# Performance work log

Measured on AMD Instinct MI355X. Metric: run time of the kernel, lower is better.

## Reference

```python
import jax, jax.numpy as jnp
import numpy as np

B, S, HID, H = 2, 2048, 2048, 16
D = HID // H  # 128 head dim
SCALE = 1.0 / np.sqrt(D)


def setup_inputs() -> dict:
    key = jax.random.key(0)
    ks = jax.random.split(key, 10)
    w = lambda k, shp: (jax.random.normal(k, shp, jnp.float32) * 0.02)
    x = jax.random.normal(ks[0], (B, S, HID), jnp.float32)
    mask = jnp.tril(jnp.ones((S, S), jnp.bool_))[None, None]  # causal [1,1,S,S]
    return {
        "x": x,
        "mask": mask,
        "Wq": w(ks[1], (HID, HID)), "bq": w(ks[2], (HID,)),
        "Wk": w(ks[3], (D, HID)),   "bk": w(ks[4], (D,)),
        "Wv": w(ks[5], (D, HID)),   "bv": w(ks[6], (D,)),
        "Wo": w(ks[7], (HID, HID)), "bo": w(ks[8], (HID,)),
    }


def reference(x, mask, Wq, bq, Wk, bk, Wv, bv, Wo, bo):
    b, s, _ = x.shape
    # projections (torch Linear: x @ W.T + b)
    q = (x @ Wq.T + bq).reshape(b, s, H, D).transpose(0, 2, 1, 3)  # [B,H,S,D]
    k = x @ Wk.T + bk  # [B,S,D] single KV head
    v = x @ Wv.T + bv  # [B,S,D]
    scores = jnp.einsum("bhqd,bkd->bhqk", q, k) * SCALE  # [B,H,S,S]
    scores = jnp.where(mask, scores, -jnp.inf)
    attn = jax.nn.softmax(scores, axis=-1)
    out = jnp.einsum("bhqk,bkd->bhqd", attn, v)  # [B,H,S,D]
    out = out.transpose(0, 2, 1, 3).reshape(b, s, HID)
    return out @ Wo.T + bo
```

## Files before the change

### kernel.cpp

```cpp
#include <hip/hip_runtime.h>


#define S_LEN 2048
#define HID_  2048
#define D_    128
#define NQKV  2304

typedef __attribute__((ext_vector_type(8))) short bf16x8;
typedef __attribute__((ext_vector_type(4))) float f32x4;
typedef __attribute__((ext_vector_type(16))) float f32x16;

__device__ __forceinline__ unsigned short f2b(float f) {
  union { float f; unsigned int u; } a; a.f = f;
  unsigned int u = a.u;
  return (unsigned short)((u + 0x7fffu + ((u >> 16) & 1u)) >> 16);
}

__device__ __forceinline__ float b2f(unsigned short s) {
  union { unsigned int u; float f; } a; a.u = ((unsigned int)s) << 16;
  return a.f;
}

__device__ __forceinline__ void load_lds16(const void* g, void* l) {
  __builtin_amdgcn_global_load_lds(
      (const __attribute__((address_space(1))) void*)g,
      (__attribute__((address_space(3))) void*)l, 16, 0, 0);
}

__device__ __forceinline__ f32x4 mfma16(bf16x8 a, bf16x8 b, f32x4 c) {
  return __builtin_amdgcn_mfma_f32_16x16x32_bf16(a, b, c, 0, 0, 0);
}

__device__ __forceinline__ f32x16 mfma32(bf16x8 a, bf16x8 b, f32x16 c) {
  return __builtin_amdgcn_mfma_f32_32x32x16_bf16(a, b, c, 0, 0, 0);
}

__device__ __forceinline__ unsigned int cvtpk(float lo, float hi) {
  unsigned int r;
  asm volatile("v_cvt_pk_bf16_f32 %0, %1, %2" : "=v"(r) : "v"(lo), "v"(hi));
  return r;
}


__global__ void cast_f32_bf16_k(const float* __restrict__ in,
                                unsigned short* __restrict__ out, int n4) {
  const int idx = blockIdx.x * 256 + threadIdx.x;
  if (idx < n4) {
    const float4 v = ((const float4*)in)[idx];
    ushort4 o;
    o.x = f2b(v.x); o.y = f2b(v.y); o.z = f2b(v.z); o.w = f2b(v.w);
    ((ushort4*)out)[idx] = o;
  }
}

__global__ void build_wcat_k(const float* __restrict__ Wq,
                             const float* __restrict__ Wk,
                             const float* __restrict__ Wv,
                             const float* __restrict__ bq,
                             const float* __restrict__ bk,
                             const float* __restrict__ bv,
                             unsigned short* __restrict__ Wcat,
                             float* __restrict__ bcat,
                             float* __restrict__ Kmax) {
  const int idx = blockIdx.x * 256 + threadIdx.x;
  const int i = idx * 4;
  const int row = i >> 11;
  const int col = i & 2047;
  const float* src;
  if (row < 2048)      src = Wq + (size_t)row * 2048 + col;
  else if (row < 2176) src = Wk + (size_t)(row - 2048) * 2048 + col;
  else                 src = Wv + (size_t)(row - 2176) * 2048 + col;
  const float4 v = *(const float4*)src;
  ushort4 o;
  o.x = f2b(v.x); o.y = f2b(v.y); o.z = f2b(v.z); o.w = f2b(v.w);
  *(ushort4*)(Wcat + i) = o;
  if (idx < NQKV)
    bcat[idx] = (idx < 2048) ? bq[idx] : (idx < 2176) ? bk[idx - 2048] : bv[idx - 2176];
  if (idx < 2) Kmax[idx] = 0.f;
}

__global__ __launch_bounds__(256)
void transpose_v(const unsigned short* __restrict__ QKV,
                 unsigned short* __restrict__ Vt) {
  __shared__ unsigned short tile[64][136];
  const int tid = threadIdx.x;
  const int s0  = blockIdx.x * 64;
  const int b   = blockIdx.y;
  const int row = tid >> 2;
  const int cb  = (tid & 3) * 32;
  const unsigned short* src = QKV + (size_t)(b * S_LEN + s0 + row) * NQKV + 2176 + cb;
#pragma unroll
  for (int i = 0; i < 4; ++i)
    *(bf16x8*)&tile[row][cb + i * 8] = *(const bf16x8*)(src + i * 8);
  __syncthreads();
  const int d  = tid >> 1;
  const int sc = (tid & 1) * 32;
  unsigned short* dst = Vt + ((size_t)b * D_ + d) * S_LEN + s0 + sc;
#pragma unroll
  for (int i = 0; i < 4; ++i) {
    bf16x8 vv;
#pragma unroll
    for (int e = 0; e < 8; ++e) vv[e] = tile[sc + i * 8 + e][d];
    *(bf16x8*)(dst + i * 8) = vv;
  }
}

__global__ __launch_bounds__(256)
void kmax_k(const unsigned short* __restrict__ QKV, float* __restrict__ Kmax) {
  __shared__ float red[256];
  const int tid = threadIdx.x;
  const int b = blockIdx.x >> 3;
  const int s = (blockIdx.x & 7) * 256 + tid;
  const unsigned short* kp = QKV + (size_t)(b * S_LEN + s) * NQKV + 2048;
  float sum = 0.f;
#pragma unroll
  for (int i = 0; i < 16; ++i) {
    bf16x8 v = *(const bf16x8*)(kp + i * 8);
#pragma unroll
    for (int e = 0; e < 8; ++e) { const float f = b2f((unsigned short)v[e]); sum += f * f; }
  }
  red[tid] = sum;
  __syncthreads();
  for (int off = 128; off > 0; off >>= 1) {
    if (tid < off) red[tid] = fmaxf(red[tid], red[tid + off]);
    __syncthreads();
  }
  if (tid == 0) atomicMax((unsigned int*)(Kmax + b), __float_as_uint(red[0]));
}


template <int OUT_F32>
__global__ __launch_bounds__(256)
void gemm_nt(const unsigned short* __restrict__ A,
             const unsigned short* __restrict__ Bm,
             const float* __restrict__ bias,
             void* __restrict__ Cv,
             int M, int N, int K) {
  __shared__ unsigned short As[128 * 32];
  __shared__ unsigned short Bs[128 * 32];
  const int tid  = threadIdx.x;
  const int lane = tid & 63;
  const int wv   = tid >> 6;
  const int wr   = wv >> 1, wc = wv & 1;
  const int g    = lane >> 4, r = lane & 15;
  const int m0   = blockIdx.y * 128;
  const int n0   = blockIdx.x * 128;

  const unsigned short* ga0 = A  + (size_t)(m0 + (tid >> 2)) * K + (tid & 3) * 8;
  const unsigned short* ga1 = ga0 + (size_t)64 * K;
  const unsigned short* gb0 = Bm + (size_t)(n0 + (tid >> 2)) * K + (tid & 3) * 8;
  const unsigned short* gb1 = gb0 + (size_t)64 * K;

  f32x4 acc[4][4] = {};

  for (int k0 = 0; k0 < K; k0 += 32) {
    __syncthreads();
    load_lds16(ga0 + k0, &As[tid * 8]);
    load_lds16(ga1 + k0, &As[2048 + tid * 8]);
    load_lds16(gb0 + k0, &Bs[tid * 8]);
    load_lds16(gb1 + k0, &Bs[2048 + tid * 8]);
    __syncthreads();
    bf16x8 af[4], bfr[4];
#pragma unroll
    for (int i = 0; i < 4; ++i)
      af[i] = *(const bf16x8*)&As[(wr * 64 + i * 16 + r) * 32 + g * 8];
#pragma unroll
    for (int i = 0; i < 4; ++i)
      bfr[i] = *(const bf16x8*)&Bs[(wc * 64 + i * 16 + r) * 32 + g * 8];
#pragma unroll
    for (int i = 0; i < 4; ++i)
#pragma unroll
      for (int j = 0; j < 4; ++j)
        acc[i][j] = mfma16(af[i], bfr[j], acc[i][j]);
  }

#pragma unroll
  for (int i = 0; i < 4; ++i) {
    const int row = m0 + wr * 64 + i * 16 + g * 4;
#pragma unroll
    for (int j = 0; j < 4; ++j) {
      const int col = n0 + wc * 64 + j * 16 + r;
      const float bb = bias[col];
#pragma unroll
      for (int e = 0; e < 4; ++e) {
        const float v = acc[i][j][e] + bb;
        if (OUT_F32) ((float*)Cv)[(size_t)(row + e) * N + col] = v;
        else ((unsigned short*)Cv)[(size_t)(row + e) * N + col] = f2b(v);
      }
    }
  }
}


__global__ __launch_bounds__(256, 2)
void mqa_attn(const unsigned short* __restrict__ QKV,
              const unsigned short* __restrict__ Vt,
              const float* __restrict__ Kmax,
              unsigned short* __restrict__ Ob) {
  __shared__ __align__(16) char Ks[2][64 * 256];
  __shared__ __align__(16) char Vs[2][64 * 256];

  const int tid  = threadIdx.x;
  const int lane = tid & 63;
  const int wv   = tid >> 6;
  const int ln   = lane & 31;
  const int hi   = lane >> 5;
  const int x    = blockIdx.x;
  const int lo   = x & 255;
  const int b    = lo >> 7;
  const int hq   = (lo >> 5) & 3;
  const int qtl  = lo & 31;
  const int qt   = (x < 256) ? qtl : 63 - qtl;
  const int h    = hq * 4 + wv;
  const int qw   = qt * 32;
  const int nt   = (qt >> 1) + 1;

  bf16x8 qf[8];
  {
    const unsigned short* qp =
        QKV + (size_t)(b * S_LEN + qw + ln) * NQKV + h * D_ + hi * 8;
#pragma unroll
    for (int ch = 0; ch < 8; ++ch) qf[ch] = *(const bf16x8*)(qp + ch * 16);
  }

  const float sscale = 0.08838834764831845f * 1.4426950408889634f;
  float qn2 = 0.f;
#pragma unroll
  for (int ch = 0; ch < 8; ++ch)
#pragma unroll
    for (int e = 0; e < 8; ++e) {
      const float qv = b2f((unsigned short)qf[ch][e]);
      qn2 += qv * qv;
    }
  qn2 += __shfl_xor(qn2, 32);
  const float m0c = sqrtf(qn2) * sqrtf(Kmax[b]) * sscale + 1.0f;

  const char* kbc = (const char*)(QKV + (size_t)(b * S_LEN) * NQKV + 2048);
  const char* vbc = (const char*)(Vt + (size_t)b * D_ * S_LEN);

  f32x16 acc[4] = {};
  float accl = 0.f;

#define STAGE(bufi, t)                                                         \
  {                                                                            \
    const int kv0_ = (t) * 64;                                                 \
    _Pragma("unroll")                                                          \
    for (int i_ = 0; i_ < 4; ++i_) {                                           \
      const int ch_ = tid + 256 * i_;                                          \
      const int kr_ = ch_ >> 4;                                                \
      const int kg_ = (ch_ & 15) ^ (kr_ & 15);                                 \
      load_lds16(kbc + (size_t)(kv0_ + kr_) * (NQKV * 2) + kg_ * 16,           \
                 Ks[bufi] + ch_ * 16);                                         \
      const int vg_ = (ch_ & 15) ^ (kr_ & 15);                                 \
      const int vd_ = kr_ * 2 + (vg_ >> 3);                                    \
      load_lds16(vbc + (size_t)vd_ * (S_LEN * 2) + kv0_ * 2 + (vg_ & 7) * 16,  \
                 Vs[bufi] + ch_ * 16);                                         \
    }                                                                          \
  }

  STAGE(0, 0);
  int cur = 0;

  for (int t = 0; t < nt; ++t) {
    __syncthreads();
    if (t + 1 < nt) STAGE(cur ^ 1, t + 1);

    const char* ksb = Ks[cur];
    const char* vsb = Vs[cur];
    const int kv0 = t * 64;
    const bool last = (t == nt - 1);
    const bool doUp = (kv0 + 32 <= qw + 31);
    cur ^= 1;

    f32x16 s0 = {}, s1 = {};
    __builtin_amdgcn_s_setprio(1);
#pragma unroll
    for (int ch = 0; ch < 8; ++ch) {
      const int slot0 = (2 * ch + hi) ^ (ln & 15);
      const bf16x8 kf0 = *(const bf16x8*)(ksb + ln * 256 + slot0 * 16);
      s0 = mfma32(kf0, qf[ch], s0);
      if (doUp) {
        const bf16x8 kf1 = *(const bf16x8*)(ksb + (32 + ln) * 256 + slot0 * 16);
        s1 = mfma32(kf1, qf[ch], s1);
      }
    }
    __builtin_amdgcn_s_setprio(0);

    bf16x8 pa0, pa1, pa2, pa3;
    float p[16];

#define SOFTMAX(sv, kvtbase)                                                   \
    _Pragma("unroll")                                                          \
    for (int r = 0; r < 16; ++r) {                                             \
      float e = sv[r] * sscale - m0c;                                          \
      if (last) {                                                              \
        const int kva = (kvtbase) + (r & 3) + 8 * (r >> 2) + 4 * hi;           \
        e = (kva <= qw + ln) ? e : -__builtin_inff();                          \
      }                                                                        \
      const float pv_ = __builtin_amdgcn_exp2f(e);                             \
      p[r] = pv_; accl += pv_;                                                 \
    }

#define PACK2(fa, fb)                                                          \
    {                                                                          \
      const unsigned int A0 = cvtpk(p[0], p[1]),   A1 = cvtpk(p[2], p[3]);     \
      const unsigned int B0 = cvtpk(p[4], p[5]),   B1 = cvtpk(p[6], p[7]);     \
      const unsigned int C0 = cvtpk(p[8], p[9]),   C1 = cvtpk(p[10], p[11]);   \
      const unsigned int D0 = cvtpk(p[12], p[13]), D1 = cvtpk(p[14], p[15]);   \
      unsigned int X0 = hi ? A0 : B0, X1 = hi ? A1 : B1;                       \
      unsigned int Y0 = hi ? C0 : D0, Y1 = hi ? C1 : D1;                       \
      X0 = (unsigned int)__shfl_xor((int)X0, 32);                              \
      X1 = (unsigned int)__shfl_xor((int)X1, 32);                              \
      Y0 = (unsigned int)__shfl_xor((int)Y0, 32);                              \
      Y1 = (unsigned int)__shfl_xor((int)Y1, 32);                              \
      union { unsigned int w[4]; bf16x8 v; } ua, ub;                           \
      ua.w[0] = hi ? X0 : A0; ua.w[1] = hi ? X1 : A1;                          \
      ua.w[2] = hi ? B0 : X0; ua.w[3] = hi ? B1 : X1;                          \
      ub.w[0] = hi ? Y0 : C0; ub.w[1] = hi ? Y1 : C1;                          \
      ub.w[2] = hi ? D0 : Y0; ub.w[3] = hi ? D1 : Y1;                          \
      fa = ua.v; fb = ub.v;                                                    \
    }

    SOFTMAX(s0, kv0)
    PACK2(pa0, pa1)
    if (doUp) {
      SOFTMAX(s1, kv0 + 32)
      PACK2(pa2, pa3)
    }

    __builtin_amdgcn_s_setprio(1);
#pragma unroll
    for (int dt = 0; dt < 4; ++dt) {
      const int vrow = dt * 16 + (ln >> 1);
      const int gb   = (ln & 1) << 3;
      {
        const int sl = (gb + 0 + hi) ^ (vrow & 15);
        const bf16x8 vf = *(const bf16x8*)(vsb + vrow * 256 + sl * 16);
        acc[dt] = mfma32(pa0, vf, acc[dt]);
      }
      {
        const int sl = (gb + 2 + hi) ^ (vrow & 15);
        const bf16x8 vf = *(const bf16x8*)(vsb + vrow * 256 + sl * 16);
        acc[dt] = mfma32(pa1, vf, acc[dt]);
      }
      if (doUp) {
        {
          const int sl = (gb + 4 + hi) ^ (vrow & 15);
          const bf16x8 vf = *(const bf16x8*)(vsb + vrow * 256 + sl * 16);
          acc[dt] = mfma32(pa2, vf, acc[dt]);
        }
        {
          const int sl = (gb + 6 + hi) ^ (vrow & 15);
          const bf16x8 vf = *(const bf16x8*)(vsb + vrow * 256 + sl * 16);
          acc[dt] = mfma32(pa3, vf, acc[dt]);
        }
      }
    }
    __builtin_amdgcn_s_setprio(0);
#undef SOFTMAX
#undef PACK2
  }

  const float lf = accl + __shfl_xor(accl, 32);
  const float linv = 1.0f / lf;
  unsigned short* ob = Ob + (size_t)(b * S_LEN + qw) * HID_ + h * D_ + ln;
#pragma unroll
  for (int r = 0; r < 16; ++r) {
    const int qr = (r & 3) + 8 * (r >> 2) + 4 * hi;
    const float li = __shfl(linv, qr);
#pragma unroll
    for (int dt = 0; dt < 4; ++dt)
      ob[(size_t)qr * HID_ + dt * 32] = f2b(acc[dt][r] * li);
  }
#undef STAGE
}


extern "C" void kernel_launch(void* const* d_in, const int* in_sizes, int n_in,
                              void* d_out, int out_size, void* d_ws, size_t ws_size,
                              hipStream_t stream) {
  (void)in_sizes; (void)n_in; (void)out_size; (void)ws_size;
  const float* x  = (const float*)d_in[0];
  const float* Wq = (const float*)d_in[2];
  const float* bq = (const float*)d_in[3];
  const float* Wk = (const float*)d_in[4];
  const float* bk = (const float*)d_in[5];
  const float* Wv = (const float*)d_in[6];
  const float* bv = (const float*)d_in[7];
  const float* Wo = (const float*)d_in[8];
  const float* bo = (const float*)d_in[9];
  float* out = (float*)d_out;

  char* p = (char*)d_ws;
  unsigned short* xb   = (unsigned short*)p;  p += (size_t)4096 * 2048 * 2;
  unsigned short* Wcat = (unsigned short*)p;  p += (size_t)2304 * 2048 * 2;
  float*          bcat = (float*)p;           p += 16384;
  unsigned short* Wob  = (unsigned short*)p;  p += (size_t)2048 * 2048 * 2;
  unsigned short* QKV  = (unsigned short*)p;  p += (size_t)4096 * 2304 * 2;
  unsigned short* Vt   = (unsigned short*)p;  p += (size_t)2 * 128 * 2048 * 2;
  float*          Kmax = (float*)p;           p += 64;
  unsigned short* Ob   = xb;

  cast_f32_bf16_k<<<8192, 256, 0, stream>>>(x, xb, 2097152);
  build_wcat_k<<<4608, 256, 0, stream>>>(Wq, Wk, Wv, bq, bk, bv, Wcat, bcat, Kmax);
  cast_f32_bf16_k<<<4096, 256, 0, stream>>>(Wo, Wob, 1048576);
  gemm_nt<0><<<dim3(18, 32), 256, 0, stream>>>(xb, Wcat, bcat, QKV, 4096, NQKV, 2048);
  transpose_v<<<dim3(32, 2), 256, 0, stream>>>(QKV, Vt);
  kmax_k<<<16, 256, 0, stream>>>(QKV, Kmax);
  mqa_attn<<<512, 256, 0, stream>>>(QKV, Vt, Kmax, Ob);
  gemm_nt<1><<<dim3(16, 32), 256, 0, stream>>>(Ob, Wob, bo, out, 4096, 2048, 2048);
}
```

Before: 215.4 us.

## Rewrite projection GEMMs with triple-buffered LDS pipeline, larger tiles and swizzle

```diff
diff --git a/kernel.cpp b/kernel.cpp
--- a/kernel.cpp
+++ b/kernel.cpp
@@ -129,57 +129,127 @@
 }
 
 
-template <int OUT_F32>
-__global__ __launch_bounds__(256)
-void gemm_nt(const unsigned short* __restrict__ A,
-             const unsigned short* __restrict__ Bm,
-             const float* __restrict__ bias,
-             void* __restrict__ Cv,
-             int M, int N, int K) {
-  __shared__ unsigned short As[128 * 32];
-  __shared__ unsigned short Bs[128 * 32];
+template <int OUT_F32, int NJ>
+__global__ __launch_bounds__(512, 2)
+void gemm_nt2(const unsigned short* __restrict__ A,
+              const unsigned short* __restrict__ Bm,
+              const float* __restrict__ bias,
+              void* __restrict__ Cv,
+              int N, int K) {
+  constexpr int BN = 64 * NJ;
+  __shared__ __align__(16) char As[3][128 * 128];
+  __shared__ __align__(16) char Bs[3][BN * 128];
+
   const int tid  = threadIdx.x;
   const int lane = tid & 63;
   const int wv   = tid >> 6;
-  const int wr   = wv >> 1, wc = wv & 1;
+  const int wr   = wv >> 2;
+  const int wc   = wv & 3;
   const int g    = lane >> 4, r = lane & 15;
-  const int m0   = blockIdx.y * 128;
-  const int n0   = blockIdx.x * 128;
-
-  const unsigned short* ga0 = A  + (size_t)(m0 + (tid >> 2)) * K + (tid & 3) * 8;
-  const unsigned short* ga1 = ga0 + (size_t)64 * K;
-  const unsigned short* gb0 = Bm + (size_t)(n0 + (tid >> 2)) * K + (tid & 3) * 8;
-  const unsigned short* gb1 = gb0 + (size_t)64 * K;
-
-  f32x4 acc[4][4] = {};
-
-  for (int k0 = 0; k0 < K; k0 += 32) {
-    __syncthreads();
-    load_lds16(ga0 + k0, &As[tid * 8]);
-    load_lds16(ga1 + k0, &As[2048 + tid * 8]);
-    load_lds16(gb0 + k0, &Bs[tid * 8]);
-    load_lds16(gb1 + k0, &Bs[2048 + tid * 8]);
-    __syncthreads();
-    bf16x8 af[4], bfr[4];
+
+  const int nwg  = gridDim.x;
+  const int bid  = blockIdx.x;
+  const int sbid = (bid & 7) * (nwg >> 3) + (bid >> 3);
+  const int nx   = N / BN;
+  const int m0   = (sbid / nx) * 128;
+  const int n0   = (sbid % nx) * BN;
+  const int NT   = K >> 6;
+
+  const size_t Kb = (size_t)K * 2;
+  const char* Ab = (const char*)A + (size_t)m0 * Kb;
+  const char* Bb = (const char*)Bm + (size_t)n0 * Kb;
+
+#define STAGE_A(bufi, t)                                                       \
+  {                                                                            \
+    const int kb_ = (t) * 128;                                                 \
+    _Pragma("unroll")                                                          \
+    for (int i_ = 0; i_ < 2; ++i_) {                                           \
+      const int ch_ = tid + 512 * i_;                                          \
+      const int rr_ = ch_ >> 3;                                                \
+      const int sl_ = (ch_ & 7) ^ (rr_ & 7);                                   \
+      load_lds16(Ab + (size_t)rr_ * Kb + kb_ + sl_ * 16, As[bufi] + ch_ * 16); \
+    }                                                                          \
+  }
+#define STAGE_B(bufi, t)                                                       \
+  {                                                                            \
+    const int kb_ = (t) * 128;                                                 \
+    _Pragma("unroll")                                                          \
+    for (int i_ = 0; i_ < NJ; ++i_) {                                          \
+      const int ch_ = tid + 512 * i_;                                          \
+      const int rr_ = ch_ >> 3;                                                \
+      const int sl_ = (ch_ & 7) ^ (rr_ & 7);                                   \
+      load_lds16(Bb + (size_t)rr_ * Kb + kb_ + sl_ * 16, Bs[bufi] + ch_ * 16); \
+    }                                                                          \
+  }
+
+  f32x4 acc[4][NJ] = {};
+  const int s0 = ((g ^ (r & 7)) << 4);
+  const int s1 = (((4 | g) ^ (r & 7)) << 4);
+
+  STAGE_A(0, 0) STAGE_B(0, 0) STAGE_A(1, 1) STAGE_B(1, 1)
+
+  asm volatile("s_waitcnt vmcnt(%0)" :: "i"(NJ + 2) : "memory");
+  __builtin_amdgcn_s_barrier();
+  __builtin_amdgcn_sched_barrier(0);
+
+  for (int t = 0; t < NT; ++t) {
+    const char* as = As[t % 3];
+    const char* bs = Bs[t % 3];
+    const int nb = (t + 2) % 3;
+    const bool pf = (t + 2 < NT);
+
+    bf16x8 af[4], bfr[NJ];
 #pragma unroll
     for (int i = 0; i < 4; ++i)
-      af[i] = *(const bf16x8*)&As[(wr * 64 + i * 16 + r) * 32 + g * 8];
+      af[i] = *(const bf16x8*)(as + ((wr * 64 + i * 16 + r) << 7) + s0);
+#pragma unroll
+    for (int j = 0; j < NJ; ++j)
+      bfr[j] = *(const bf16x8*)(bs + ((wc * 16 * NJ + j * 16 + r) << 7) + s0);
+    if (pf) STAGE_A(nb, t + 2)
+    __builtin_amdgcn_s_barrier();
+    __builtin_amdgcn_sched_barrier(0);
+    asm volatile("s_waitcnt lgkmcnt(0)" ::: "memory");
+    __builtin_amdgcn_sched_barrier(0);
+    __builtin_amdgcn_s_setprio(1);
 #pragma unroll
     for (int i = 0; i < 4; ++i)
-      bfr[i] = *(const bf16x8*)&Bs[(wc * 64 + i * 16 + r) * 32 + g * 8];
+#pragma unroll
+      for (int j = 0; j < NJ; ++j)
+        acc[i][j] = mfma16(af[i], bfr[j], acc[i][j]);
+    __builtin_amdgcn_s_setprio(0);
+    __builtin_amdgcn_sched_barrier(0);
+
 #pragma unroll
     for (int i = 0; i < 4; ++i)
-#pragma unroll
-      for (int j = 0; j < 4; ++j)
+      af[i] = *(const bf16x8*)(as + ((wr * 64 + i * 16 + r) << 7) + s1);
+#pragma unroll
+    for (int j = 0; j < NJ; ++j)
+      bfr[j] = *(const bf16x8*)(bs + ((wc * 16 * NJ + j * 16 + r) << 7) + s1);
+    if (pf) STAGE_B(nb, t + 2)
+    __builtin_amdgcn_s_barrier();
+    __builtin_amdgcn_sched_barrier(0);
+    asm volatile("s_waitcnt lgkmcnt(0)" ::: "memory");
+    __builtin_amdgcn_sched_barrier(0);
+    __builtin_amdgcn_s_setprio(1);
+#pragma unroll
+    for (int i = 0; i < 4; ++i)
+#pragma unroll
+      for (int j = 0; j < NJ; ++j)
         acc[i][j] = mfma16(af[i], bfr[j], acc[i][j]);
+    __builtin_amdgcn_s_setprio(0);
+
+    if (pf) { asm volatile("s_waitcnt vmcnt(%0)" :: "i"(NJ + 2) : "memory"); }
+    else    { asm volatile("s_waitcnt vmcnt(0)" ::: "memory"); }
+    __builtin_amdgcn_s_barrier();
+    __builtin_amdgcn_sched_barrier(0);
   }
 
 #pragma unroll
   for (int i = 0; i < 4; ++i) {
     const int row = m0 + wr * 64 + i * 16 + g * 4;
 #pragma unroll
-    for (int j = 0; j < 4; ++j) {
-      const int col = n0 + wc * 64 + j * 16 + r;
+    for (int j = 0; j < NJ; ++j) {
+      const int col = n0 + wc * 16 * NJ + j * 16 + r;
       const float bb = bias[col];
 #pragma unroll
       for (int e = 0; e < 4; ++e) {
@@ -189,6 +259,8 @@
       }
     }
   }
+#undef STAGE_A
+#undef STAGE_B
 }
 
 
@@ -272,16 +344,16 @@
     const bool doUp = (kv0 + 32 <= qw + 31);
     cur ^= 1;
 
-    f32x16 s0 = {}, s1 = {};
+    f32x16 sA = {}, sB = {};
     __builtin_amdgcn_s_setprio(1);
 #pragma unroll
     for (int ch = 0; ch < 8; ++ch) {
       const int slot0 = (2 * ch + hi) ^ (ln & 15);
       const bf16x8 kf0 = *(const bf16x8*)(ksb + ln * 256 + slot0 * 16);
-      s0 = mfma32(kf0, qf[ch], s0);
+      sA = mfma32(kf0, qf[ch], sA);
       if (doUp) {
         const bf16x8 kf1 = *(const bf16x8*)(ksb + (32 + ln) * 256 + slot0 * 16);
-        s1 = mfma32(kf1, qf[ch], s1);
+        sB = mfma32(kf1, qf[ch], sB);
       }
     }
     __builtin_amdgcn_s_setprio(0);
@@ -291,14 +363,14 @@
 
 #define SOFTMAX(sv, kvtbase)                                                   \
     _Pragma("unroll")                                                          \
-    for (int r = 0; r < 16; ++r) {                                             \
-      float e = sv[r] * sscale - m0c;                                          \
+    for (int rr = 0; rr < 16; ++rr) {                                          \
+      float e = sv[rr] * sscale - m0c;                                         \
       if (last) {                                                              \
-        const int kva = (kvtbase) + (r & 3) + 8 * (r >> 2) + 4 * hi;           \
+        const int kva = (kvtbase) + (rr & 3) + 8 * (rr >> 2) + 4 * hi;         \
         e = (kva <= qw + ln) ? e : -__builtin_inff();                          \
       }                                                                        \
       const float pv_ = __builtin_amdgcn_exp2f(e);                             \
-      p[r] = pv_; accl += pv_;                                                 \
+      p[rr] = pv_; accl += pv_;                                                \
     }
 
 #define PACK2(fa, fb)                                                          \
@@ -321,10 +393,10 @@
       fa = ua.v; fb = ub.v;                                                    \
     }
 
-    SOFTMAX(s0, kv0)
+    SOFTMAX(sA, kv0)
     PACK2(pa0, pa1)
     if (doUp) {
-      SOFTMAX(s1, kv0 + 32)
+      SOFTMAX(sB, kv0 + 32)
       PACK2(pa2, pa3)
     }
 
@@ -365,12 +437,12 @@
   const float linv = 1.0f / lf;
   unsigned short* ob = Ob + (size_t)(b * S_LEN + qw) * HID_ + h * D_ + ln;
 #pragma unroll
-  for (int r = 0; r < 16; ++r) {
-    const int qr = (r & 3) + 8 * (r >> 2) + 4 * hi;
+  for (int rr = 0; rr < 16; ++rr) {
+    const int qr = (rr & 3) + 8 * (rr >> 2) + 4 * hi;
     const float li = __shfl(linv, qr);
 #pragma unroll
     for (int dt = 0; dt < 4; ++dt)
-      ob[(size_t)qr * HID_ + dt * 32] = f2b(acc[dt][r] * li);
+      ob[(size_t)qr * HID_ + dt * 32] = f2b(acc[dt][rr] * li);
   }
 #undef STAGE
 }
@@ -404,9 +476,9 @@
   cast_f32_bf16_k<<<8192, 256, 0, stream>>>(x, xb, 2097152);
   build_wcat_k<<<4608, 256, 0, stream>>>(Wq, Wk, Wv, bq, bk, bv, Wcat, bcat, Kmax);
   cast_f32_bf16_k<<<4096, 256, 0, stream>>>(Wo, Wob, 1048576);
-  gemm_nt<0><<<dim3(18, 32), 256, 0, stream>>>(xb, Wcat, bcat, QKV, 4096, NQKV, 2048);
+  gemm_nt2<0, 3><<<384, 512, 0, stream>>>(xb, Wcat, bcat, QKV, 2304, 2048);
   transpose_v<<<dim3(32, 2), 256, 0, stream>>>(QKV, Vt);
   kmax_k<<<16, 256, 0, stream>>>(QKV, Kmax);
   mqa_attn<<<512, 256, 0, stream>>>(QKV, Vt, Kmax, Ob);
-  gemm_nt<1><<<dim3(16, 32), 256, 0, stream>>>(Ob, Wob, bo, out, 4096, 2048, 2048);
-}
+  gemm_nt2<1, 4><<<256, 512, 0, stream>>>(Ob, Wob, bo, out, 2048, 2048);
+}
```

New measurement: 199.2 us. -7.5%, faster.
